# Kernel tuning notes

Measured on AMD Instinct MI355X. Metric: run time of the kernel, lower is better.

Reference implementation:

```python
import jax, jax.numpy as jnp
import numpy as np

H, W = 16, 16
DIM = 512
HEADS = 8
DIM_HEAD = 64
INNER = HEADS * DIM_HEAD  # 512
B = 8
N = H * W  # 256
SCALE = DIM_HEAD ** -0.5
EPS = 1e-5


def _index_map(h, w):
    # index_map[n, m] = dx * (2w-1) + dy with dx = x-i+h-1, dy = y-j+w-1
    xs = np.arange(h)
    ys = np.arange(w)
    dx = xs[:, None] - xs[None, :] + h - 1            # (h, h)
    dy = ys[:, None] - ys[None, :] + w - 1            # (w, w)
    idx = dx[:, None, :, None] * (2 * w - 1) + dy[None, :, None, :]  # (h, w, h, w)
    return idx.reshape(h * w, h * w).astype(np.int32)


def setup_inputs() -> dict:
    key = jax.random.key(0)
    ks = jax.random.split(key, 5)
    x = jax.random.normal(ks[0], (B, N, DIM), dtype=jnp.float32)
    ln_g = jnp.ones((DIM,), jnp.float32)
    ln_b = jnp.zeros((DIM,), jnp.float32)
    w_qkv = jax.random.normal(ks[1], (DIM, 3 * INNER), jnp.float32) * 0.02
    unique_params = jax.random.normal(ks[2], ((2 * H - 1) * (2 * W - 1), INNER), jnp.float32) * 0.02
    w_out = jax.random.normal(ks[3], (INNER, DIM), jnp.float32) * 0.02
    b_out = jnp.zeros((DIM,), jnp.float32)
    idx_map = jnp.asarray(_index_map(H, W))  # (N, N) int32
    return {"x": x, "ln_g": ln_g, "ln_b": ln_b, "w_qkv": w_qkv,
            "unique_params": unique_params, "w_out": w_out, "b_out": b_out,
            "idx_map": idx_map}


def reference(x, ln_g, ln_b, w_qkv, unique_params, w_out, b_out, idx_map):
    b, n, _ = x.shape
    # LayerNorm
    mu = jnp.mean(x, axis=-1, keepdims=True)
    var = jnp.mean(jnp.square(x - mu), axis=-1, keepdims=True)
    xn = (x - mu) * jax.lax.rsqrt(var + EPS) * ln_g + ln_b
    # qkv projection (no bias)
    qkv = xn @ w_qkv                                  # (b, n, 3*inner)
    q, k, v = jnp.split(qkv, 3, axis=-1)
    q = q.reshape(b, n, HEADS, DIM_HEAD)
    k = k.reshape(b, n, HEADS, DIM_HEAD)
    v = v.reshape(b, n, HEADS, DIM_HEAD)
    # attention scores
    dots = jnp.einsum('bnhd,bmhd->bhnm', q, k) * SCALE
    attn = jax.nn.softmax(dots, axis=-1)              # (b, h, n, m)
    # relative-position table: (n, m, h, d)
    rpos = unique_params[idx_map].reshape(n, n, HEADS, DIM_HEAD)
    # out[b,h,n,d] = sum_m attn[b,h,n,m] * (v[b,m,h,d] + rpos[n,m,h,d])
    out = jnp.einsum('bhnm,bmhd->bnhd', attn, v) \
        + jnp.einsum('bhnm,nmhd->bnhd', attn, rpos)
    out = out.reshape(b, n, INNER)
    return out @ w_out + b_out
```

## Files before the change

### kernel.cpp

```cpp
#include <hip/hip_runtime.h>
#include <math.h>

#define NB 8
#define SEQ 256
#define DIMC 512
#define NHEAD 8
#define DHEAD 64
#define SCALEF 0.125f

typedef __attribute__((ext_vector_type(8))) short s16x8;
typedef __attribute__((ext_vector_type(4))) float f32x4;

typedef __attribute__((address_space(3))) unsigned int lds_u32_t;
typedef const __attribute__((address_space(1))) unsigned int g_u32_t;
static __device__ __forceinline__ void gl_lds16(const void* gsrc, void* ldst) {
  __builtin_amdgcn_global_load_lds((g_u32_t*)gsrc, (lds_u32_t*)ldst, 16, 0, 0);
}

static __device__ __forceinline__ unsigned short f2bf(float f) {
  union { float f; unsigned u; } c; c.f = f;
  unsigned r = c.u + 0x7FFF + ((c.u >> 16) & 1);
  return (unsigned short)(r >> 16);
}
static __device__ __forceinline__ float bf2f(unsigned short u) {
  union { unsigned u; float f; } c; c.u = ((unsigned)u) << 16;
  return c.f;
}

static __device__ void tcast_body(const float* __restrict__ W,
    unsigned short* __restrict__ WT, int K, int N, int n0, int k0, int t,
    float (*tile)[65]) {
#pragma unroll
  for (int i = 0; i < 16; ++i) {
    const int idx = i * 256 + t;
    const int kl = idx >> 6, nl = idx & 63;
    tile[kl][nl] = W[(size_t)(k0 + kl) * N + n0 + nl];
  }
  __syncthreads();
#pragma unroll
  for (int i = 0; i < 16; ++i) {
    const int idx = i * 256 + t;
    const int nl = idx >> 6, kl = idx & 63;
    WT[(size_t)(n0 + nl) * K + k0 + kl] = f2bf(tile[kl][nl]);
  }
}

__global__ __launch_bounds__(256) void prep_kernel(const float* __restrict__ x,
    const float* __restrict__ g, const float* __restrict__ bta,
    const float* __restrict__ w_qkv, unsigned short* __restrict__ xnb,
    unsigned short* __restrict__ wqt) {
  __shared__ float tile[64][65];
  __shared__ float sh_s[4], sh_q[4];
  const int t = threadIdx.x;
  const int bid = blockIdx.x;
  if (bid < 192) {
    tcast_body(w_qkv, wqt, 512, 1536, (bid % 24) * 64, (bid / 24) * 64, t, tile);
  } else {
    const int row = bid - 192;
    const float2 v = ((const float2*)(x + (size_t)row * DIMC))[t];
    float s = v.x + v.y;
    float q = v.x * v.x + v.y * v.y;
#pragma unroll
    for (int off = 32; off > 0; off >>= 1) {
      s += __shfl_down(s, off);
      q += __shfl_down(q, off);
    }
    const int wave = t >> 6, lane = t & 63;
    if (lane == 0) { sh_s[wave] = s; sh_q[wave] = q; }
    __syncthreads();
    const float fs = sh_s[0] + sh_s[1] + sh_s[2] + sh_s[3];
    const float fq = sh_q[0] + sh_q[1] + sh_q[2] + sh_q[3];
    const float mean = fs * (1.0f / DIMC);
    const float inv = rsqrtf(fq * (1.0f / DIMC) - mean * mean + 1e-5f);
    const float2 gv = ((const float2*)g)[t];
    const float2 bv = ((const float2*)bta)[t];
    ushort2 o;
    o.x = f2bf((v.x - mean) * inv * gv.x + bv.x);
    o.y = f2bf((v.y - mean) * inv * gv.y + bv.y);
    ((ushort2*)(xnb + (size_t)row * DIMC))[t] = o;
  }
}

template <int BM, int BN, bool BIAS, bool OUTBF, bool VSPLIT, bool TAIL>
__global__ __launch_bounds__(256) void gemm64_kernel(
    const unsigned short* __restrict__ A, const unsigned short* __restrict__ BT,
    const float* __restrict__ bias, void* __restrict__ Cv,
    unsigned short* __restrict__ vtb, int M, int K, int N, int nbm,
    const float* __restrict__ w_out, unsigned short* __restrict__ wot,
    const float* __restrict__ up, unsigned short* __restrict__ upb) {
  constexpr int ABYTES = (BM * 64 + BN * 64) * 2;
  constexpr int LDSZ = TAIL ? (ABYTES > 16640 ? ABYTES : 16640) : ABYTES;
  __shared__ alignas(16) unsigned char smem[LDSZ];
  unsigned short* As = (unsigned short*)smem;
  unsigned short* Bs = As + BM * 64;
  const int t = threadIdx.x;
  const int bid = blockIdx.x;
  const int gemmBlocks = nbm * (N / BN);

  if constexpr (TAIL) {
    if (bid >= gemmBlocks) {
      const int b2 = bid - gemmBlocks;
      if (b2 < 64) {
        float (*tile)[65] = (float(*)[65])smem;
        tcast_body(w_out, wot, 512, 512, (b2 % 8) * 64, (b2 / 8) * 64, t, tile);
      } else {
        const int base = (b2 - 64) * 2048 + t * 4;
#pragma unroll
        for (int it = 0; it < 2; ++it) {
          const int i = base + it * 1024;
          if (i < 492032) {
            const float4 v = *(const float4*)&up[i];
            ushort4 w;
            w.x = f2bf(v.x); w.y = f2bf(v.y); w.z = f2bf(v.z); w.w = f2bf(v.w);
            *(ushort4*)&upb[i] = w;
          }
        }
      }
      return;
    }
  }

  constexpr int TR = BM / 32;
  constexpr int TC = BN / 32;
  const int wave = t >> 6, lane = t & 63;
  const int wr = wave >> 1, wc = wave & 1;
  const int bm = (bid % nbm) * BM, bn = (bid / nbm) * BN;
  const int fr = lane & 15, q4 = lane >> 4;

  f32x4 acc[TR][TC] = {};

  const int kBlocks = K >> 6;
  for (int kb = 0; kb < kBlocks; ++kb) {
    const int k0 = kb << 6;
    __syncthreads();
#pragma unroll
    for (int c = 0; c < BM * 8 / 256; ++c) {
      const int p = c * 256 + t;
      const int row = p >> 3;
      const int jl = (p & 7) ^ (row & 7);
      gl_lds16(A + (size_t)(bm + row) * K + k0 + jl * 8,
               As + (size_t)(c * 256 + wave * 64) * 8);
    }
#pragma unroll
    for (int c = 0; c < BN * 8 / 256; ++c) {
      const int p = c * 256 + t;
      const int row = p >> 3;
      const int jl = (p & 7) ^ (row & 7);
      gl_lds16(BT + (size_t)(bn + row) * K + k0 + jl * 8,
               Bs + (size_t)(c * 256 + wave * 64) * 8);
    }
    __syncthreads();
    s16x8 af[TR][2], bfr[TC][2];
#pragma unroll
    for (int i = 0; i < TR; ++i)
#pragma unroll
      for (int ks = 0; ks < 2; ++ks) {
        const int row = wr * (BM / 2) + i * 16 + fr;
        const int jp = (ks * 4 + q4) ^ (fr & 7);
        af[i][ks] = *(const s16x8*)(As + row * 64 + jp * 8);
      }
#pragma unroll
    for (int j = 0; j < TC; ++j)
#pragma unroll
      for (int ks = 0; ks < 2; ++ks) {
        const int row = wc * (BN / 2) + j * 16 + fr;
        const int jp = (ks * 4 + q4) ^ (fr & 7);
        bfr[j][ks] = *(const s16x8*)(Bs + row * 64 + jp * 8);
      }
#pragma unroll
    for (int ks = 0; ks < 2; ++ks)
#pragma unroll
      for (int i = 0; i < TR; ++i)
#pragma unroll
        for (int j = 0; j < TC; ++j)
          acc[i][j] = __builtin_amdgcn_mfma_f32_16x16x32_bf16(
              af[i][ks], bfr[j][ks], acc[i][j], 0, 0, 0);
  }
  if (VSPLIT && bn >= 1024) {
#pragma unroll
    for (int i = 0; i < TR; ++i) {
#pragma unroll
      for (int j = 0; j < TC; ++j) {
        const int hc = bn - 1024 + wc * (BN / 2) + j * 16 + fr;
        const int h = hc >> 6, d = hc & 63;
#pragma unroll
        for (int r = 0; r < 4; ++r) {
          const int row = bm + wr * (BM / 2) + i * 16 + q4 * 4 + r;
          const int b = row >> 8, m = row & 255;
          vtb[(size_t)((b * 8 + h) * 64 + d) * 256 + m] = f2bf(acc[i][j][r]);
        }
      }
    }
    return;
  }
#pragma unroll
  for (int i = 0; i < TR; ++i) {
#pragma unroll
    for (int j = 0; j < TC; ++j) {
      const int col = bn + wc * (BN / 2) + j * 16 + fr;
      const float bv = BIAS ? bias[col] : 0.0f;
#pragma unroll
      for (int r = 0; r < 4; ++r) {
        const int row = bm + wr * (BM / 2) + i * 16 + q4 * 4 + r;
        if constexpr (OUTBF) {
          ((unsigned short*)Cv)[(size_t)row * N + col] = f2bf(acc[i][j][r] + bv);
        } else {
          ((float*)Cv)[(size_t)row * N + col] = acc[i][j][r] + bv;
        }
      }
    }
  }
}

#define PSTR 264
#define KSTR 72
__global__ __launch_bounds__(128) void fused_attn_kernel(
    const unsigned short* __restrict__ qkvb, const unsigned short* __restrict__ vtb,
    unsigned short* __restrict__ attnb, unsigned short* __restrict__ oav) {
  __shared__ unsigned short kv_lds[256 * KSTR];
  __shared__ unsigned short p_lds[32 * PSTR];
  const int bh = blockIdx.y, b = bh >> 3, h = bh & 7;
  const int n0 = blockIdx.x * 32;
  const int t = threadIdx.x, wave = t >> 6, lane = t & 63;
  const int fr = lane & 15, q4 = lane >> 4;

#pragma unroll
  for (int p = 0; p < 16; ++p) {
    const int chunk = p * 128 + t;
    const int m = chunk >> 3, c = chunk & 7;
    *(s16x8*)(kv_lds + m * KSTR + c * 8) =
        *(const s16x8*)(qkvb + (size_t)(b * SEQ + m) * 1536 + 512 + h * 64 + c * 8);
  }
  s16x8 qf[2];
  {
    const size_t qrow = (size_t)(b * SEQ + n0 + wave * 16 + fr) * 1536 + h * 64;
#pragma unroll
    for (int ks = 0; ks < 2; ++ks)
      qf[ks] = *(const s16x8*)(qkvb + qrow + ks * 32 + q4 * 8);
  }
  __syncthreads();

  f32x4 s[16];
#pragma unroll
  for (int mt = 0; mt < 16; ++mt) s[mt] = (f32x4){0.f, 0.f, 0.f, 0.f};
#pragma unroll
  for (int ks = 0; ks < 2; ++ks)
#pragma unroll
    for (int mt = 0; mt < 16; ++mt) {
      const s16x8 kf =
          *(const s16x8*)(kv_lds + (mt * 16 + fr) * KSTR + ks * 32 + q4 * 8);
      s[mt] = __builtin_amdgcn_mfma_f32_16x16x32_bf16(qf[ks], kf, s[mt], 0, 0, 0);
    }

  float mx[4] = {-1e30f, -1e30f, -1e30f, -1e30f};
#pragma unroll
  for (int mt = 0; mt < 16; ++mt)
#pragma unroll
    for (int r = 0; r < 4; ++r) {
      s[mt][r] *= SCALEF;
      mx[r] = fmaxf(mx[r], s[mt][r]);
    }
#pragma unroll
  for (int r = 0; r < 4; ++r) {
    mx[r] = fmaxf(mx[r], __shfl_xor(mx[r], 1));
    mx[r] = fmaxf(mx[r], __shfl_xor(mx[r], 2));
    mx[r] = fmaxf(mx[r], __shfl_xor(mx[r], 4));
    mx[r] = fmaxf(mx[r], __shfl_xor(mx[r], 8));
  }
  float sum[4] = {0.f, 0.f, 0.f, 0.f};
#pragma unroll
  for (int mt = 0; mt < 16; ++mt)
#pragma unroll
    for (int r = 0; r < 4; ++r) {
      s[mt][r] = __expf(s[mt][r] - mx[r]);
      sum[r] += s[mt][r];
    }
#pragma unroll
  for (int r = 0; r < 4; ++r) {
    sum[r] += __shfl_xor(sum[r], 1);
    sum[r] += __shfl_xor(sum[r], 2);
    sum[r] += __shfl_xor(sum[r], 4);
    sum[r] += __shfl_xor(sum[r], 8);
  }
  const float invs[4] = {1.0f / sum[0], 1.0f / sum[1], 1.0f / sum[2],
                         1.0f / sum[3]};

  __syncthreads();

  {
    const int nb = wave * 16 + q4 * 4;
#pragma unroll
    for (int mt = 0; mt < 16; ++mt)
#pragma unroll
      for (int r = 0; r < 4; ++r)
        p_lds[(nb + r) * PSTR + mt * 16 + fr] = f2bf(s[mt][r] * invs[r]);
  }
#pragma unroll
  for (int p = 0; p < 16; ++p) {
    const int idx = p * 128 + t;
    const int d = idx >> 5, c = idx & 31;
    *(s16x8*)(kv_lds + d * PSTR + c * 8) =
        *(const s16x8*)(vtb + (size_t)(bh * 64 + d) * 256 + c * 8);
  }
  __syncthreads();

#pragma unroll
  for (int p = 0; p < 8; ++p) {
    const int idx = p * 128 + t;
    const int row = idx >> 5, mc = (idx & 31) * 8;
    *(s16x8*)(attnb + (size_t)(bh * SEQ + n0 + row) * SEQ + mc) =
        *(const s16x8*)(p_lds + row * PSTR + mc);
  }

  f32x4 o[4];
#pragma unroll
  for (int dt = 0; dt < 4; ++dt) o[dt] = (f32x4){0.f, 0.f, 0.f, 0.f};
#pragma unroll
  for (int ks = 0; ks < 8; ++ks) {
    const s16x8 pf =
        *(const s16x8*)(p_lds + (wave * 16 + fr) * PSTR + ks * 32 + q4 * 8);
#pragma unroll
    for (int dt = 0; dt < 4; ++dt) {
      const s16x8 vf =
          *(const s16x8*)(kv_lds + (dt * 16 + fr) * PSTR + ks * 32 + q4 * 8);
      o[dt] = __builtin_amdgcn_mfma_f32_16x16x32_bf16(pf, vf, o[dt], 0, 0, 0);
    }
  }
#pragma unroll
  for (int dt = 0; dt < 4; ++dt)
#pragma unroll
    for (int r = 0; r < 4; ++r) {
      const int n = n0 + wave * 16 + q4 * 4 + r;
      oav[(size_t)(b * SEQ + n) * DIMC + h * 64 + dt * 16 + fr] = f2bf(o[dt][r]);
    }
}

#define RSTRIDE 280
__global__ __launch_bounds__(256) void rpos_kernel(
    const unsigned short* __restrict__ attnb, const unsigned short* __restrict__ upb,
    unsigned short* __restrict__ ob) {
  __shared__ float aS[4][4 * RSTRIDE];
  const int t = threadIdx.x;
  const int wave = t >> 6, lane = t & 63;
  const int idx = blockIdx.x * 4 + wave;
  const int bhalf = idx & 1;
  const int h = (idx >> 1) & 7;
  const int n = idx >> 4;
  float* aW = aS[wave];

  const int m4 = lane * 4;
  const int sm4 = m4 + ((m4 >> 6) << 3);
#pragma unroll
  for (int bl = 0; bl < 4; ++bl) {
    const int b = bhalf * 4 + bl;
    const ushort4 v =
        *(const ushort4*)&attnb[(size_t)((b * 8 + h) * SEQ + n) * SEQ + m4];
    float4 f;
    f.x = bf2f(v.x); f.y = bf2f(v.y); f.z = bf2f(v.z); f.w = bf2f(v.w);
    *(float4*)&aW[bl * RSTRIDE + sm4] = f;
  }
  __syncthreads();

  const int g = lane >> 3, dl = lane & 7;
  const int xn = n >> 4, yn = n & 15;
  float acc[4][8];
#pragma unroll
  for (int bl = 0; bl < 4; ++bl)
#pragma unroll
    for (int j = 0; j < 8; ++j) acc[bl][j] = 0.0f;

  const int sbase = g * 32 + (g >> 1) * 8;
#pragma unroll 4
  for (int mm = 0; mm < 32; ++mm) {
    const int m = g * 32 + mm;
    const int xm = m >> 4, ym = m & 15;
    const int row = (xn - xm + 15) * 31 + (yn - ym + 15);
    const s16x8 uv = *(const s16x8*)(upb + (size_t)row * DIMC + h * 64 + dl * 8);
    float uf[8];
#pragma unroll
    for (int j = 0; j < 8; ++j) uf[j] = bf2f((unsigned short)uv[j]);
    float ab[4];
#pragma unroll
    for (int bl = 0; bl < 4; ++bl) ab[bl] = aW[bl * RSTRIDE + sbase + mm];
#pragma unroll
    for (int bl = 0; bl < 4; ++bl)
#pragma unroll
      for (int j = 0; j < 8; ++j) acc[bl][j] += ab[bl] * uf[j];
  }
#pragma unroll
  for (int bl = 0; bl < 4; ++bl)
#pragma unroll
    for (int j = 0; j < 8; ++j) {
      float v = acc[bl][j];
      v += __shfl_xor(v, 8);
      v += __shfl_xor(v, 16);
      v += __shfl_xor(v, 32);
      acc[bl][j] = v;
    }
  if (g < 4) {
    const int b = bhalf * 4 + g;
    unsigned short* p = ob + (size_t)(b * SEQ + n) * DIMC + h * 64 + dl * 8;
    s16x8 pv = *(s16x8*)p;
    s16x8 w;
#pragma unroll
    for (int j = 0; j < 8; ++j)
      w[j] = (short)f2bf(bf2f((unsigned short)pv[j]) + acc[g][j]);
    *(s16x8*)p = w;
  }
}

extern "C" void kernel_launch(void* const* d_in, const int* in_sizes, int n_in,
                              void* d_out, int out_size, void* d_ws,
                              size_t ws_size, hipStream_t stream) {
  const float* x = (const float*)d_in[0];
  const float* ln_g = (const float*)d_in[1];
  const float* ln_b = (const float*)d_in[2];
  const float* w_qkv = (const float*)d_in[3];
  const float* up = (const float*)d_in[4];
  const float* w_out = (const float*)d_in[5];
  const float* b_out = (const float*)d_in[6];
  float* out = (float*)d_out;

  unsigned short* u = (unsigned short*)d_ws;
  unsigned short* qkvb = u;
  unsigned short* attnb = u + 3145728;
  unsigned short* xnb = u + 7340032;
  unsigned short* ob = u + 8388608;
  unsigned short* wqt = u + 9437184;
  unsigned short* wot = u + 10223616;
  unsigned short* upb = u + 10485760;
  unsigned short* vtb = u + 10977792;
  if (ws_size < (size_t)12026368 * sizeof(unsigned short)) return;

  prep_kernel<<<2240, 256, 0, stream>>>(x, ln_g, ln_b, w_qkv, xnb, wqt);
  gemm64_kernel<64, 64, false, true, true, true>
      <<<1073, 256, 0, stream>>>(xnb, wqt, nullptr, qkvb, vtb, 2048, 512, 1536,
                                 32, w_out, wot, up, upb);
  fused_attn_kernel<<<dim3(8, 64), 128, 0, stream>>>(qkvb, vtb, attnb, ob);
  rpos_kernel<<<1024, 256, 0, stream>>>(attnb, upb, ob);
  gemm64_kernel<64, 32, true, false, false, false>
      <<<512, 256, 0, stream>>>(ob, wot, b_out, out, nullptr, 2048, 512, 512,
                                32, nullptr, nullptr, nullptr, nullptr);
}
```

Measured before the change: 120.7 us.

## Merge all stages into one cooperative persistent kernel with grid syncs

Replaces the five separate launches (prep, QKV GEMM, attention, rpos, output GEMM) with one cooperative kernel of 256 blocks that loops over tasks per stage and separates stages with grid.sync. Attention tiles grow to 64 query rows per 256-thread block, and the output GEMM now uses 64x64 tiles. The goal is to remove launch gaps between kernels. In exchange, only 256 blocks run, each with about 70KB of LDS, so occupancy is low, and every stage pays for a grid-wide barrier.

```diff
diff --git a/kernel.cpp b/kernel.cpp
--- a/kernel.cpp
+++ b/kernel.cpp
@@ -1,12 +1,15 @@
 #include <hip/hip_runtime.h>
+#include <hip/hip_cooperative_groups.h>
 #include <math.h>
 
-#define NB 8
+namespace cg = cooperative_groups;
+
 #define SEQ 256
 #define DIMC 512
-#define NHEAD 8
-#define DHEAD 64
 #define SCALEF 0.125f
+#define PSTR 264
+#define KSTR 72
+#define RSTRIDE 280
 
 typedef __attribute__((ext_vector_type(8))) short s16x8;
 typedef __attribute__((ext_vector_type(4))) float f32x4;
@@ -27,9 +30,10 @@
   return c.f;
 }
 
-static __device__ void tcast_body(const float* __restrict__ W,
+static __device__ void tcast_tile(const float* __restrict__ W,
     unsigned short* __restrict__ WT, int K, int N, int n0, int k0, int t,
-    float (*tile)[65]) {
+    unsigned char* smem) {
+  float (*tile)[65] = (float(*)[65])smem;
 #pragma unroll
   for (int i = 0; i < 16; ++i) {
     const int idx = i * 256 + t;
@@ -43,98 +47,26 @@
     const int nl = idx >> 6, kl = idx & 63;
     WT[(size_t)(n0 + nl) * K + k0 + kl] = f2bf(tile[kl][nl]);
   }
-}
-
-__global__ __launch_bounds__(256) void prep_kernel(const float* __restrict__ x,
-    const float* __restrict__ g, const float* __restrict__ bta,
-    const float* __restrict__ w_qkv, unsigned short* __restrict__ xnb,
-    unsigned short* __restrict__ wqt) {
-  __shared__ float tile[64][65];
-  __shared__ float sh_s[4], sh_q[4];
-  const int t = threadIdx.x;
-  const int bid = blockIdx.x;
-  if (bid < 192) {
-    tcast_body(w_qkv, wqt, 512, 1536, (bid % 24) * 64, (bid / 24) * 64, t, tile);
-  } else {
-    const int row = bid - 192;
-    const float2 v = ((const float2*)(x + (size_t)row * DIMC))[t];
-    float s = v.x + v.y;
-    float q = v.x * v.x + v.y * v.y;
-#pragma unroll
-    for (int off = 32; off > 0; off >>= 1) {
-      s += __shfl_down(s, off);
-      q += __shfl_down(q, off);
-    }
-    const int wave = t >> 6, lane = t & 63;
-    if (lane == 0) { sh_s[wave] = s; sh_q[wave] = q; }
-    __syncthreads();
-    const float fs = sh_s[0] + sh_s[1] + sh_s[2] + sh_s[3];
-    const float fq = sh_q[0] + sh_q[1] + sh_q[2] + sh_q[3];
-    const float mean = fs * (1.0f / DIMC);
-    const float inv = rsqrtf(fq * (1.0f / DIMC) - mean * mean + 1e-5f);
-    const float2 gv = ((const float2*)g)[t];
-    const float2 bv = ((const float2*)bta)[t];
-    ushort2 o;
-    o.x = f2bf((v.x - mean) * inv * gv.x + bv.x);
-    o.y = f2bf((v.y - mean) * inv * gv.y + bv.y);
-    ((ushort2*)(xnb + (size_t)row * DIMC))[t] = o;
-  }
-}
-
-template <int BM, int BN, bool BIAS, bool OUTBF, bool VSPLIT, bool TAIL>
-__global__ __launch_bounds__(256) void gemm64_kernel(
-    const unsigned short* __restrict__ A, const unsigned short* __restrict__ BT,
-    const float* __restrict__ bias, void* __restrict__ Cv,
-    unsigned short* __restrict__ vtb, int M, int K, int N, int nbm,
-    const float* __restrict__ w_out, unsigned short* __restrict__ wot,
-    const float* __restrict__ up, unsigned short* __restrict__ upb) {
-  constexpr int ABYTES = (BM * 64 + BN * 64) * 2;
-  constexpr int LDSZ = TAIL ? (ABYTES > 16640 ? ABYTES : 16640) : ABYTES;
-  __shared__ alignas(16) unsigned char smem[LDSZ];
+  __syncthreads();
+}
+
+template <bool OUTBF, bool BIAS, bool VSPLIT>
+static __device__ void gemm_tile(const unsigned short* __restrict__ A,
+    const unsigned short* __restrict__ BT, const float* __restrict__ bias,
+    void* __restrict__ Cv, unsigned short* __restrict__ vtb,
+    int bm, int bn, int K, int N, int t, unsigned char* smem) {
   unsigned short* As = (unsigned short*)smem;
-  unsigned short* Bs = As + BM * 64;
-  const int t = threadIdx.x;
-  const int bid = blockIdx.x;
-  const int gemmBlocks = nbm * (N / BN);
-
-  if constexpr (TAIL) {
-    if (bid >= gemmBlocks) {
-      const int b2 = bid - gemmBlocks;
-      if (b2 < 64) {
-        float (*tile)[65] = (float(*)[65])smem;
-        tcast_body(w_out, wot, 512, 512, (b2 % 8) * 64, (b2 / 8) * 64, t, tile);
-      } else {
-        const int base = (b2 - 64) * 2048 + t * 4;
-#pragma unroll
-        for (int it = 0; it < 2; ++it) {
-          const int i = base + it * 1024;
-          if (i < 492032) {
-            const float4 v = *(const float4*)&up[i];
-            ushort4 w;
-            w.x = f2bf(v.x); w.y = f2bf(v.y); w.z = f2bf(v.z); w.w = f2bf(v.w);
-            *(ushort4*)&upb[i] = w;
-          }
-        }
-      }
-      return;
-    }
-  }
-
-  constexpr int TR = BM / 32;
-  constexpr int TC = BN / 32;
+  unsigned short* Bs = As + 64 * 64;
   const int wave = t >> 6, lane = t & 63;
   const int wr = wave >> 1, wc = wave & 1;
-  const int bm = (bid % nbm) * BM, bn = (bid / nbm) * BN;
   const int fr = lane & 15, q4 = lane >> 4;
-
-  f32x4 acc[TR][TC] = {};
-
+  f32x4 acc[2][2] = {};
   const int kBlocks = K >> 6;
   for (int kb = 0; kb < kBlocks; ++kb) {
     const int k0 = kb << 6;
     __syncthreads();
 #pragma unroll
-    for (int c = 0; c < BM * 8 / 256; ++c) {
+    for (int c = 0; c < 2; ++c) {
       const int p = c * 256 + t;
       const int row = p >> 3;
       const int jl = (p & 7) ^ (row & 7);
@@ -142,7 +74,7 @@
                As + (size_t)(c * 256 + wave * 64) * 8);
     }
 #pragma unroll
-    for (int c = 0; c < BN * 8 / 256; ++c) {
+    for (int c = 0; c < 2; ++c) {
       const int p = c * 256 + t;
       const int row = p >> 3;
       const int jl = (p & 7) ^ (row & 7);
@@ -150,58 +82,57 @@
                Bs + (size_t)(c * 256 + wave * 64) * 8);
     }
     __syncthreads();
-    s16x8 af[TR][2], bfr[TC][2];
-#pragma unroll
-    for (int i = 0; i < TR; ++i)
+    s16x8 af[2][2], bfr[2][2];
+#pragma unroll
+    for (int i = 0; i < 2; ++i)
 #pragma unroll
       for (int ks = 0; ks < 2; ++ks) {
-        const int row = wr * (BM / 2) + i * 16 + fr;
+        const int row = wr * 32 + i * 16 + fr;
         const int jp = (ks * 4 + q4) ^ (fr & 7);
         af[i][ks] = *(const s16x8*)(As + row * 64 + jp * 8);
       }
 #pragma unroll
-    for (int j = 0; j < TC; ++j)
+    for (int j = 0; j < 2; ++j)
 #pragma unroll
       for (int ks = 0; ks < 2; ++ks) {
-        const int row = wc * (BN / 2) + j * 16 + fr;
+        const int row = wc * 32 + j * 16 + fr;
         const int jp = (ks * 4 + q4) ^ (fr & 7);
         bfr[j][ks] = *(const s16x8*)(Bs + row * 64 + jp * 8);
       }
 #pragma unroll
     for (int ks = 0; ks < 2; ++ks)
 #pragma unroll
-      for (int i = 0; i < TR; ++i)
-#pragma unroll
-        for (int j = 0; j < TC; ++j)
+      for (int i = 0; i < 2; ++i)
+#pragma unroll
+        for (int j = 0; j < 2; ++j)
           acc[i][j] = __builtin_amdgcn_mfma_f32_16x16x32_bf16(
               af[i][ks], bfr[j][ks], acc[i][j], 0, 0, 0);
   }
   if (VSPLIT && bn >= 1024) {
 #pragma unroll
-    for (int i = 0; i < TR; ++i) {
-#pragma unroll
-      for (int j = 0; j < TC; ++j) {
-        const int hc = bn - 1024 + wc * (BN / 2) + j * 16 + fr;
+    for (int i = 0; i < 2; ++i)
+#pragma unroll
+      for (int j = 0; j < 2; ++j) {
+        const int hc = bn - 1024 + wc * 32 + j * 16 + fr;
         const int h = hc >> 6, d = hc & 63;
 #pragma unroll
         for (int r = 0; r < 4; ++r) {
-          const int row = bm + wr * (BM / 2) + i * 16 + q4 * 4 + r;
+          const int row = bm + wr * 32 + i * 16 + q4 * 4 + r;
           const int b = row >> 8, m = row & 255;
           vtb[(size_t)((b * 8 + h) * 64 + d) * 256 + m] = f2bf(acc[i][j][r]);
         }
       }
-    }
     return;
   }
 #pragma unroll
-  for (int i = 0; i < TR; ++i) {
-#pragma unroll
-    for (int j = 0; j < TC; ++j) {
-      const int col = bn + wc * (BN / 2) + j * 16 + fr;
+  for (int i = 0; i < 2; ++i)
+#pragma unroll
+    for (int j = 0; j < 2; ++j) {
+      const int col = bn + wc * 32 + j * 16 + fr;
       const float bv = BIAS ? bias[col] : 0.0f;
 #pragma unroll
       for (int r = 0; r < 4; ++r) {
-        const int row = bm + wr * (BM / 2) + i * 16 + q4 * 4 + r;
+        const int row = bm + wr * 32 + i * 16 + q4 * 4 + r;
         if constexpr (OUTBF) {
           ((unsigned short*)Cv)[(size_t)row * N + col] = f2bf(acc[i][j][r] + bv);
         } else {
@@ -209,204 +140,268 @@
         }
       }
     }
-  }
-}
-
-#define PSTR 264
-#define KSTR 72
-__global__ __launch_bounds__(128) void fused_attn_kernel(
-    const unsigned short* __restrict__ qkvb, const unsigned short* __restrict__ vtb,
-    unsigned short* __restrict__ attnb, unsigned short* __restrict__ oav) {
-  __shared__ unsigned short kv_lds[256 * KSTR];
-  __shared__ unsigned short p_lds[32 * PSTR];
-  const int bh = blockIdx.y, b = bh >> 3, h = bh & 7;
-  const int n0 = blockIdx.x * 32;
-  const int t = threadIdx.x, wave = t >> 6, lane = t & 63;
+}
+
+__global__ __launch_bounds__(256) void mega_kernel(
+    const float* __restrict__ x, const float* __restrict__ g,
+    const float* __restrict__ bta, const float* __restrict__ w_qkv,
+    const float* __restrict__ w_out, const float* __restrict__ b_out,
+    const float* __restrict__ up, float* __restrict__ out,
+    unsigned short* __restrict__ xnb, unsigned short* __restrict__ wqt,
+    unsigned short* __restrict__ wot, unsigned short* __restrict__ upb,
+    unsigned short* __restrict__ qkvb, unsigned short* __restrict__ vtb,
+    unsigned short* __restrict__ attnb, unsigned short* __restrict__ ob) {
+  cg::grid_group grid = cg::this_grid();
+  __shared__ alignas(16) unsigned char smem[70656];
+  const int t = threadIdx.x;
+  const int bid = blockIdx.x;
+  const int wave = t >> 6, lane = t & 63;
   const int fr = lane & 15, q4 = lane >> 4;
 
-#pragma unroll
-  for (int p = 0; p < 16; ++p) {
-    const int chunk = p * 128 + t;
-    const int m = chunk >> 3, c = chunk & 7;
-    *(s16x8*)(kv_lds + m * KSTR + c * 8) =
-        *(const s16x8*)(qkvb + (size_t)(b * SEQ + m) * 1536 + 512 + h * 64 + c * 8);
-  }
-  s16x8 qf[2];
+  for (int task = bid; task < 2545; task += 256) {
+    if (task < 192) {
+      tcast_tile(w_qkv, wqt, 512, 1536, (task % 24) * 64, (task / 24) * 64, t, smem);
+    } else if (task < 256) {
+      const int b2 = task - 192;
+      tcast_tile(w_out, wot, 512, 512, (b2 % 8) * 64, (b2 / 8) * 64, t, smem);
+    } else if (task < 497) {
+      const int base = (task - 256) * 2048 + t * 4;
+#pragma unroll
+      for (int it = 0; it < 2; ++it) {
+        const int i = base + it * 1024;
+        if (i < 492032) {
+          const float4 v = *(const float4*)&up[i];
+          ushort4 w;
+          w.x = f2bf(v.x); w.y = f2bf(v.y); w.z = f2bf(v.z); w.w = f2bf(v.w);
+          *(ushort4*)&upb[i] = w;
+        }
+      }
+    } else {
+      const int row = task - 497;
+      float* sh = (float*)smem;
+      const float2 v = ((const float2*)(x + (size_t)row * DIMC))[t];
+      float s = v.x + v.y;
+      float q = v.x * v.x + v.y * v.y;
+#pragma unroll
+      for (int off = 32; off > 0; off >>= 1) {
+        s += __shfl_down(s, off);
+        q += __shfl_down(q, off);
+      }
+      if (lane == 0) { sh[wave] = s; sh[4 + wave] = q; }
+      __syncthreads();
+      const float fs = sh[0] + sh[1] + sh[2] + sh[3];
+      const float fq = sh[4] + sh[5] + sh[6] + sh[7];
+      const float mean = fs * (1.0f / DIMC);
+      const float inv = rsqrtf(fq * (1.0f / DIMC) - mean * mean + 1e-5f);
+      const float2 gv = ((const float2*)g)[t];
+      const float2 bv = ((const float2*)bta)[t];
+      ushort2 o;
+      o.x = f2bf((v.x - mean) * inv * gv.x + bv.x);
+      o.y = f2bf((v.y - mean) * inv * gv.y + bv.y);
+      ((ushort2*)(xnb + (size_t)row * DIMC))[t] = o;
+      __syncthreads();
+    }
+  }
+  grid.sync();
+
+#pragma unroll
+  for (int tt = 0; tt < 3; ++tt) {
+    const int tile = bid + tt * 256;
+    gemm_tile<true, false, true>(xnb, wqt, nullptr, qkvb, vtb,
+                                 (tile & 31) * 64, (tile >> 5) * 64,
+                                 512, 1536, t, smem);
+  }
+  grid.sync();
+
   {
+    unsigned short* kv_lds = (unsigned short*)smem;
+    unsigned short* p_lds = kv_lds + 256 * KSTR;
+    const int bh = bid >> 2, b = bh >> 3, h = bh & 7;
+    const int n0 = (bid & 3) * 64;
+
+    const int dc = (t & 7) * 8;
+#pragma unroll
+    for (int p = 0; p < 8; ++p) {
+      const int m = p * 32 + (t >> 3);
+      *(s16x8*)(kv_lds + m * KSTR + dc) =
+          *(const s16x8*)(qkvb + (size_t)(b * SEQ + m) * 1536 + 512 + h * 64 + dc);
+    }
+    s16x8 qf[2];
     const size_t qrow = (size_t)(b * SEQ + n0 + wave * 16 + fr) * 1536 + h * 64;
 #pragma unroll
     for (int ks = 0; ks < 2; ++ks)
       qf[ks] = *(const s16x8*)(qkvb + qrow + ks * 32 + q4 * 8);
-  }
-  __syncthreads();
-
-  f32x4 s[16];
-#pragma unroll
-  for (int mt = 0; mt < 16; ++mt) s[mt] = (f32x4){0.f, 0.f, 0.f, 0.f};
-#pragma unroll
-  for (int ks = 0; ks < 2; ++ks)
-#pragma unroll
-    for (int mt = 0; mt < 16; ++mt) {
-      const s16x8 kf =
-          *(const s16x8*)(kv_lds + (mt * 16 + fr) * KSTR + ks * 32 + q4 * 8);
-      s[mt] = __builtin_amdgcn_mfma_f32_16x16x32_bf16(qf[ks], kf, s[mt], 0, 0, 0);
-    }
-
-  float mx[4] = {-1e30f, -1e30f, -1e30f, -1e30f};
-#pragma unroll
-  for (int mt = 0; mt < 16; ++mt)
+    __syncthreads();
+
+    f32x4 s[16];
+#pragma unroll
+    for (int mt = 0; mt < 16; ++mt) s[mt] = (f32x4){0.f, 0.f, 0.f, 0.f};
+#pragma unroll
+    for (int ks = 0; ks < 2; ++ks)
+#pragma unroll
+      for (int mt = 0; mt < 16; ++mt) {
+        const s16x8 kf =
+            *(const s16x8*)(kv_lds + (mt * 16 + fr) * KSTR + ks * 32 + q4 * 8);
+        s[mt] = __builtin_amdgcn_mfma_f32_16x16x32_bf16(qf[ks], kf, s[mt], 0, 0, 0);
+      }
+
+    float mx[4] = {-1e30f, -1e30f, -1e30f, -1e30f};
+#pragma unroll
+    for (int mt = 0; mt < 16; ++mt)
+#pragma unroll
+      for (int r = 0; r < 4; ++r) {
+        s[mt][r] *= SCALEF;
+        mx[r] = fmaxf(mx[r], s[mt][r]);
+      }
 #pragma unroll
     for (int r = 0; r < 4; ++r) {
-      s[mt][r] *= SCALEF;
-      mx[r] = fmaxf(mx[r], s[mt][r]);
-    }
-#pragma unroll
-  for (int r = 0; r < 4; ++r) {
-    mx[r] = fmaxf(mx[r], __shfl_xor(mx[r], 1));
-    mx[r] = fmaxf(mx[r], __shfl_xor(mx[r], 2));
-    mx[r] = fmaxf(mx[r], __shfl_xor(mx[r], 4));
-    mx[r] = fmaxf(mx[r], __shfl_xor(mx[r], 8));
-  }
-  float sum[4] = {0.f, 0.f, 0.f, 0.f};
-#pragma unroll
-  for (int mt = 0; mt < 16; ++mt)
+      mx[r] = fmaxf(mx[r], __shfl_xor(mx[r], 1));
+      mx[r] = fmaxf(mx[r], __shfl_xor(mx[r], 2));
+      mx[r] = fmaxf(mx[r], __shfl_xor(mx[r], 4));
+      mx[r] = fmaxf(mx[r], __shfl_xor(mx[r], 8));
+    }
+    float sum[4] = {0.f, 0.f, 0.f, 0.f};
+#pragma unroll
+    for (int mt = 0; mt < 16; ++mt)
+#pragma unroll
+      for (int r = 0; r < 4; ++r) {
+        s[mt][r] = __expf(s[mt][r] - mx[r]);
+        sum[r] += s[mt][r];
+      }
 #pragma unroll
     for (int r = 0; r < 4; ++r) {
-      s[mt][r] = __expf(s[mt][r] - mx[r]);
-      sum[r] += s[mt][r];
-    }
-#pragma unroll
-  for (int r = 0; r < 4; ++r) {
-    sum[r] += __shfl_xor(sum[r], 1);
-    sum[r] += __shfl_xor(sum[r], 2);
-    sum[r] += __shfl_xor(sum[r], 4);
-    sum[r] += __shfl_xor(sum[r], 8);
-  }
-  const float invs[4] = {1.0f / sum[0], 1.0f / sum[1], 1.0f / sum[2],
-                         1.0f / sum[3]};
-
-  __syncthreads();
+      sum[r] += __shfl_xor(sum[r], 1);
+      sum[r] += __shfl_xor(sum[r], 2);
+      sum[r] += __shfl_xor(sum[r], 4);
+      sum[r] += __shfl_xor(sum[r], 8);
+    }
+    const float invs[4] = {1.0f / sum[0], 1.0f / sum[1], 1.0f / sum[2],
+                           1.0f / sum[3]};
+    __syncthreads();
+
+    {
+      const int nb = wave * 16 + q4 * 4;
+#pragma unroll
+      for (int mt = 0; mt < 16; ++mt)
+#pragma unroll
+        for (int r = 0; r < 4; ++r)
+          p_lds[(nb + r) * PSTR + mt * 16 + fr] = f2bf(s[mt][r] * invs[r]);
+    }
+#pragma unroll
+    for (int p = 0; p < 8; ++p) {
+      const int idx = p * 256 + t;
+      const int d = idx >> 5, c = idx & 31;
+      *(s16x8*)(kv_lds + d * PSTR + c * 8) =
+          *(const s16x8*)(vtb + (size_t)(bh * 64 + d) * 256 + c * 8);
+    }
+    __syncthreads();
+
+#pragma unroll
+    for (int p = 0; p < 8; ++p) {
+      const int idx = p * 256 + t;
+      const int row = idx >> 5, mc = (idx & 31) * 8;
+      *(s16x8*)(attnb + (size_t)(bh * SEQ + n0 + row) * SEQ + mc) =
+          *(const s16x8*)(p_lds + row * PSTR + mc);
+    }
+
+    f32x4 o[4];
+#pragma unroll
+    for (int dt = 0; dt < 4; ++dt) o[dt] = (f32x4){0.f, 0.f, 0.f, 0.f};
+#pragma unroll
+    for (int ks = 0; ks < 8; ++ks) {
+      const s16x8 pf =
+          *(const s16x8*)(p_lds + (wave * 16 + fr) * PSTR + ks * 32 + q4 * 8);
+#pragma unroll
+      for (int dt = 0; dt < 4; ++dt) {
+        const s16x8 vf =
+            *(const s16x8*)(kv_lds + (dt * 16 + fr) * PSTR + ks * 32 + q4 * 8);
+        o[dt] = __builtin_amdgcn_mfma_f32_16x16x32_bf16(pf, vf, o[dt], 0, 0, 0);
+      }
+    }
+#pragma unroll
+    for (int dt = 0; dt < 4; ++dt)
+#pragma unroll
+      for (int r = 0; r < 4; ++r) {
+        const int n = n0 + wave * 16 + q4 * 4 + r;
+        ob[(size_t)(b * SEQ + n) * DIMC + h * 64 + dt * 16 + fr] = f2bf(o[dt][r]);
+      }
+  }
+  grid.sync();
 
   {
-    const int nb = wave * 16 + q4 * 4;
-#pragma unroll
-    for (int mt = 0; mt < 16; ++mt)
-#pragma unroll
-      for (int r = 0; r < 4; ++r)
-        p_lds[(nb + r) * PSTR + mt * 16 + fr] = f2bf(s[mt][r] * invs[r]);
-  }
-#pragma unroll
-  for (int p = 0; p < 16; ++p) {
-    const int idx = p * 128 + t;
-    const int d = idx >> 5, c = idx & 31;
-    *(s16x8*)(kv_lds + d * PSTR + c * 8) =
-        *(const s16x8*)(vtb + (size_t)(bh * 64 + d) * 256 + c * 8);
-  }
-  __syncthreads();
-
-#pragma unroll
-  for (int p = 0; p < 8; ++p) {
-    const int idx = p * 128 + t;
-    const int row = idx >> 5, mc = (idx & 31) * 8;
-    *(s16x8*)(attnb + (size_t)(bh * SEQ + n0 + row) * SEQ + mc) =
-        *(const s16x8*)(p_lds + row * PSTR + mc);
-  }
-
-  f32x4 o[4];
-#pragma unroll
-  for (int dt = 0; dt < 4; ++dt) o[dt] = (f32x4){0.f, 0.f, 0.f, 0.f};
-#pragma unroll
-  for (int ks = 0; ks < 8; ++ks) {
-    const s16x8 pf =
-        *(const s16x8*)(p_lds + (wave * 16 + fr) * PSTR + ks * 32 + q4 * 8);
-#pragma unroll
-    for (int dt = 0; dt < 4; ++dt) {
-      const s16x8 vf =
-          *(const s16x8*)(kv_lds + (dt * 16 + fr) * PSTR + ks * 32 + q4 * 8);
-      o[dt] = __builtin_amdgcn_mfma_f32_16x16x32_bf16(pf, vf, o[dt], 0, 0, 0);
-    }
-  }
-#pragma unroll
-  for (int dt = 0; dt < 4; ++dt)
-#pragma unroll
-    for (int r = 0; r < 4; ++r) {
-      const int n = n0 + wave * 16 + q4 * 4 + r;
-      oav[(size_t)(b * SEQ + n) * DIMC + h * 64 + dt * 16 + fr] = f2bf(o[dt][r]);
-    }
-}
-
-#define RSTRIDE 280
-__global__ __launch_bounds__(256) void rpos_kernel(
-    const unsigned short* __restrict__ attnb, const unsigned short* __restrict__ upb,
-    unsigned short* __restrict__ ob) {
-  __shared__ float aS[4][4 * RSTRIDE];
-  const int t = threadIdx.x;
-  const int wave = t >> 6, lane = t & 63;
-  const int idx = blockIdx.x * 4 + wave;
-  const int bhalf = idx & 1;
-  const int h = (idx >> 1) & 7;
-  const int n = idx >> 4;
-  float* aW = aS[wave];
-
-  const int m4 = lane * 4;
-  const int sm4 = m4 + ((m4 >> 6) << 3);
-#pragma unroll
-  for (int bl = 0; bl < 4; ++bl) {
-    const int b = bhalf * 4 + bl;
-    const ushort4 v =
-        *(const ushort4*)&attnb[(size_t)((b * 8 + h) * SEQ + n) * SEQ + m4];
-    float4 f;
-    f.x = bf2f(v.x); f.y = bf2f(v.y); f.z = bf2f(v.z); f.w = bf2f(v.w);
-    *(float4*)&aW[bl * RSTRIDE + sm4] = f;
-  }
-  __syncthreads();
-
-  const int g = lane >> 3, dl = lane & 7;
-  const int xn = n >> 4, yn = n & 15;
-  float acc[4][8];
-#pragma unroll
-  for (int bl = 0; bl < 4; ++bl)
-#pragma unroll
-    for (int j = 0; j < 8; ++j) acc[bl][j] = 0.0f;
-
-  const int sbase = g * 32 + (g >> 1) * 8;
+    float* aW = (float*)smem + wave * 4 * RSTRIDE;
+    const int m4 = lane * 4;
+    const int sm4 = m4 + ((m4 >> 6) << 3);
+    const int g8 = lane >> 3, dl = lane & 7;
+    const int sbase = g8 * 32 + (g8 >> 1) * 8;
+    for (int it = 0; it < 4; ++it) {
+      const int idx = bid * 16 + it * 4 + wave;
+      const int bhalf = idx & 1;
+      const int h = (idx >> 1) & 7;
+      const int n = idx >> 4;
+#pragma unroll
+      for (int bl = 0; bl < 4; ++bl) {
+        const int b = bhalf * 4 + bl;
+        const ushort4 v =
+            *(const ushort4*)&attnb[(size_t)((b * 8 + h) * SEQ + n) * SEQ + m4];
+        float4 f;
+        f.x = bf2f(v.x); f.y = bf2f(v.y); f.z = bf2f(v.z); f.w = bf2f(v.w);
+        *(float4*)&aW[bl * RSTRIDE + sm4] = f;
+      }
+      __syncthreads();
+
+      const int xn = n >> 4, yn = n & 15;
+      float acc[4][8];
+#pragma unroll
+      for (int bl = 0; bl < 4; ++bl)
+#pragma unroll
+        for (int j = 0; j < 8; ++j) acc[bl][j] = 0.0f;
 #pragma unroll 4
-  for (int mm = 0; mm < 32; ++mm) {
-    const int m = g * 32 + mm;
-    const int xm = m >> 4, ym = m & 15;
-    const int row = (xn - xm + 15) * 31 + (yn - ym + 15);
-    const s16x8 uv = *(const s16x8*)(upb + (size_t)row * DIMC + h * 64 + dl * 8);
-    float uf[8];
-#pragma unroll
-    for (int j = 0; j < 8; ++j) uf[j] = bf2f((unsigned short)uv[j]);
-    float ab[4];
-#pragma unroll
-    for (int bl = 0; bl < 4; ++bl) ab[bl] = aW[bl * RSTRIDE + sbase + mm];
-#pragma unroll
-    for (int bl = 0; bl < 4; ++bl)
-#pragma unroll
-      for (int j = 0; j < 8; ++j) acc[bl][j] += ab[bl] * uf[j];
-  }
-#pragma unroll
-  for (int bl = 0; bl < 4; ++bl)
-#pragma unroll
-    for (int j = 0; j < 8; ++j) {
-      float v = acc[bl][j];
-      v += __shfl_xor(v, 8);
-      v += __shfl_xor(v, 16);
-      v += __shfl_xor(v, 32);
-      acc[bl][j] = v;
-    }
-  if (g < 4) {
-    const int b = bhalf * 4 + g;
-    unsigned short* p = ob + (size_t)(b * SEQ + n) * DIMC + h * 64 + dl * 8;
-    s16x8 pv = *(s16x8*)p;
-    s16x8 w;
-#pragma unroll
-    for (int j = 0; j < 8; ++j)
-      w[j] = (short)f2bf(bf2f((unsigned short)pv[j]) + acc[g][j]);
-    *(s16x8*)p = w;
-  }
+      for (int mm = 0; mm < 32; ++mm) {
+        const int m = g8 * 32 + mm;
+        const int xm = m >> 4, ym = m & 15;
+        const int row = (xn - xm + 15) * 31 + (yn - ym + 15);
+        const s16x8 uv =
+            *(const s16x8*)(upb + (size_t)row * DIMC + h * 64 + dl * 8);
+        float uf[8];
+#pragma unroll
+        for (int j = 0; j < 8; ++j) uf[j] = bf2f((unsigned short)uv[j]);
+        float ab[4];
+#pragma unroll
+        for (int bl = 0; bl < 4; ++bl) ab[bl] = aW[bl * RSTRIDE + sbase + mm];
+#pragma unroll
+        for (int bl = 0; bl < 4; ++bl)
+#pragma unroll
+          for (int j = 0; j < 8; ++j) acc[bl][j] += ab[bl] * uf[j];
+      }
+#pragma unroll
+      for (int bl = 0; bl < 4; ++bl)
+#pragma unroll
+        for (int j = 0; j < 8; ++j) {
+          float v = acc[bl][j];
+          v += __shfl_xor(v, 8);
+          v += __shfl_xor(v, 16);
+          v += __shfl_xor(v, 32);
+          acc[bl][j] = v;
+        }
+      if (g8 < 4) {
+        const int b = bhalf * 4 + g8;
+        unsigned short* p = ob + (size_t)(b * SEQ + n) * DIMC + h * 64 + dl * 8;
+        s16x8 pv = *(s16x8*)p;
+        s16x8 w;
+#pragma unroll
+        for (int j = 0; j < 8; ++j)
+          w[j] = (short)f2bf(bf2f((unsigned short)pv[j]) + acc[g8][j]);
+        *(s16x8*)p = w;
+      }
+      __syncthreads();
+    }
+  }
+  grid.sync();
+
+  gemm_tile<false, true, false>(ob, wot, b_out, out, nullptr,
+                                (bid & 31) * 64, (bid >> 5) * 64,
+                                512, 512, t, smem);
 }
 
 extern "C" void kernel_launch(void* const* d_in, const int* in_sizes, int n_in,
@@ -432,13 +427,10 @@
   unsigned short* vtb = u + 10977792;
   if (ws_size < (size_t)12026368 * sizeof(unsigned short)) return;
 
-  prep_kernel<<<2240, 256, 0, stream>>>(x, ln_g, ln_b, w_qkv, xnb, wqt);
-  gemm64_kernel<64, 64, false, true, true, true>
-      <<<1073, 256, 0, stream>>>(xnb, wqt, nullptr, qkvb, vtb, 2048, 512, 1536,
-                                 32, w_out, wot, up, upb);
-  fused_attn_kernel<<<dim3(8, 64), 128, 0, stream>>>(qkvb, vtb, attnb, ob);
-  rpos_kernel<<<1024, 256, 0, stream>>>(attnb, upb, ob);
-  gemm64_kernel<64, 32, true, false, false, false>
-      <<<512, 256, 0, stream>>>(ob, wot, b_out, out, nullptr, 2048, 512, 512,
-                                32, nullptr, nullptr, nullptr, nullptr);
-}
+  void* args[] = {(void*)&x,    (void*)&ln_g, (void*)&ln_b, (void*)&w_qkv,
+                  (void*)&w_out, (void*)&b_out, (void*)&up,  (void*)&out,
+                  (void*)&xnb,  (void*)&wqt,  (void*)&wot,  (void*)&upb,
+                  (void*)&qkvb, (void*)&vtb,  (void*)&attnb, (void*)&ob};
+  hipLaunchCooperativeKernel((void*)mega_kernel, dim3(256), dim3(256),
+                             args, 0, stream);
+}
```

After: 267.6 us. +121.7%, slower.
